# Optimization experiments

Hardware: AMD Instinct MI355X
Metric: run time of the kernel (lower is better)

The kernel has to match this reference:

```python
import jax, jax.numpy as jnp
import numpy as np

D_MODEL = 768
N_HEADS = 12
D_K = D_MODEL // N_HEADS


def setup_inputs() -> dict:
    key = jax.random.key(0)
    ks = jax.random.split(key, 11)
    B, T = 4, 2048
    s = 1.0 / np.sqrt(D_K)
    so = 1.0 / np.sqrt(D_MODEL)
    return {
        "q": jax.random.normal(ks[0], (B, T, D_MODEL), jnp.float32),
        "k": jax.random.normal(ks[1], (B, T, D_MODEL), jnp.float32),
        "v": jax.random.normal(ks[2], (B, T, D_MODEL), jnp.float32),
        "Wq": jax.random.normal(ks[3], (D_K, D_K), jnp.float32) * s,
        "bq": jax.random.normal(ks[4], (D_K,), jnp.float32) * s,
        "Wk": jax.random.normal(ks[5], (D_K, D_K), jnp.float32) * s,
        "bk": jax.random.normal(ks[6], (D_K,), jnp.float32) * s,
        "Wv": jax.random.normal(ks[7], (D_K, D_K), jnp.float32) * s,
        "bv": jax.random.normal(ks[8], (D_K,), jnp.float32) * s,
        "Wo": jax.random.normal(ks[9], (D_MODEL, D_MODEL), jnp.float32) * so,
        "bo": jax.random.normal(ks[10], (D_MODEL,), jnp.float32) * so,
    }


def reference(q, k, v, Wq, bq, Wk, bk, Wv, bv, Wo, bo):
    B, T, _ = q.shape
    # split into heads: [B, T, H, d_k]; per-head Linear shares weights across heads
    qh = q.reshape(B, T, N_HEADS, D_K)
    kh = k.reshape(B, T, N_HEADS, D_K)
    vh = v.reshape(B, T, N_HEADS, D_K)
    # torch Linear: x @ W^T + b, then transpose to [B, H, T, d_k]
    qh = jnp.einsum("bthd,ed->bhte", qh, Wq) + bq
    kh = jnp.einsum("bthd,ed->bhte", kh, Wk) + bk
    vh = jnp.einsum("bthd,ed->bhte", vh, Wv) + bv
    # scaled dot-product attention, full [B,H,T,T] scores (faithful to source)
    scores = jnp.einsum("bhqd,bhkd->bhqk", qh, kh) / jnp.sqrt(
        jnp.asarray(D_K, qh.dtype)
    )
    attn = jax.nn.softmax(scores, axis=-1)
    # einsum 'ijkl,ijlr->ikjr' -> output laid out [B, T, H, d_k]
    out_h = jnp.einsum("bhqk,bhkd->bqhd", attn, vh)
    concat = out_h.reshape(B, T, D_MODEL)
    return concat @ Wo.T + bo
```

## Files before the change

kernel.cpp:

```cpp
#include <hip/hip_runtime.h>
#include <hip/hip_bf16.h>


#define T_SEQ  2048
#define NH     12
#define DK     64
#define DMODEL 768
#define BATCH  4

typedef __attribute__((ext_vector_type(8))) short short8;
typedef __attribute__((ext_vector_type(4))) float f32x4;
typedef __attribute__((ext_vector_type(4))) unsigned short us4;
typedef __attribute__((ext_vector_type(2))) unsigned int u32x2;

__device__ __forceinline__ unsigned short f2bf(float f) {
  union { float f; unsigned int i; } x; x.f = f;
  unsigned int r = x.i + 0x7fffu + ((x.i >> 16) & 1u);
  return (unsigned short)(r >> 16);
}
__device__ __forceinline__ us4 f4_to_bf4(float4 v) {
  us4 r; r.x = f2bf(v.x); r.y = f2bf(v.y); r.z = f2bf(v.z); r.w = f2bf(v.w); return r;
}
__device__ __forceinline__ unsigned int pack_bf2(float a, float b) {
  union { __hip_bfloat162 h; unsigned int u; } x;
  x.h = __float22bfloat162_rn(float2{a, b});
  return x.u;
}


__global__ __launch_bounds__(256, 4)
void qkv_proj_kernel(const float* __restrict__ qin,
                     const float* __restrict__ kin,
                     const float* __restrict__ vin,
                     const float* __restrict__ Wq, const float* __restrict__ bq,
                     const float* __restrict__ Wk, const float* __restrict__ bk,
                     const float* __restrict__ Wv, const float* __restrict__ bv,
                     unsigned short* __restrict__ Qp,
                     unsigned short* __restrict__ Kp,
                     unsigned short* __restrict__ Vt)
{
  const int tt  = blockIdx.x;
  const int bh  = blockIdx.y;
  const int p   = blockIdx.z;
  const int b   = bh / NH, h = bh % NH;
  const int t0  = tt * 64;
  const int tid = threadIdx.x;
  const int wv  = tid >> 6;
  const int ln  = tid & 63;
  const int c   = ln & 15;
  const int qd  = ln >> 4;

  __shared__ __align__(16) unsigned short sX[64 * 72];
  __shared__ __align__(16) unsigned short sW[64 * 72];
  __shared__ __align__(16) unsigned short sVtr[64 * 68];

  const float* in = (p == 0) ? qin : (p == 1) ? kin : vin;
  const float* W  = (p == 0) ? Wq  : (p == 1) ? Wk  : Wv;
  const float* bs = (p == 0) ? bq  : (p == 1) ? bk  : bv;

  const int r0 = tid >> 4, g = tid & 15;
#pragma unroll
  for (int l = 0; l < 4; ++l) {
    int r = l * 16 + r0;
    float4 xv = *reinterpret_cast<const float4*>(in + ((size_t)(b * T_SEQ + t0 + r)) * DMODEL + h * DK + g * 4);
    *reinterpret_cast<us4*>(&sX[r * 72 + g * 4]) = f4_to_bf4(xv);
    float4 wvv = *reinterpret_cast<const float4*>(W + r * DK + g * 4);
    *reinterpret_cast<us4*>(&sW[r * 72 + g * 4]) = f4_to_bf4(wvv);
  }
  __syncthreads();

  short8 af[2];
#pragma unroll
  for (int kc = 0; kc < 2; ++kc)
    af[kc] = *reinterpret_cast<const short8*>(&sX[(wv * 16 + c) * 72 + kc * 32 + qd * 8]);

  f32x4 acc[4];
#pragma unroll
  for (int nb = 0; nb < 4; ++nb) {
    f32x4 a = {0.f, 0.f, 0.f, 0.f};
#pragma unroll
    for (int kc = 0; kc < 2; ++kc) {
      short8 bf = *reinterpret_cast<const short8*>(&sW[(nb * 16 + c) * 72 + kc * 32 + qd * 8]);
      a = __builtin_amdgcn_mfma_f32_16x16x32_bf16(af[kc], bf, a, 0, 0, 0);
    }
    acc[nb] = a;
  }

  const float cexp = 0.125f * 1.44269504088896340736f;
  if (p < 2) {
    unsigned short* outp = (p == 0) ? Qp : Kp;
    const float mul = (p == 0) ? cexp : 1.0f;
#pragma unroll
    for (int nb = 0; nb < 4; ++nb) {
      int n = nb * 16 + c;
      float bias = bs[n];
#pragma unroll
      for (int r = 0; r < 4; ++r) {
        int t = t0 + wv * 16 + qd * 4 + r;
        outp[((size_t)bh * T_SEQ + t) * DK + n] = f2bf((acc[nb][r] + bias) * mul);
      }
    }
  } else {
#pragma unroll
    for (int nb = 0; nb < 4; ++nb) {
      int n = nb * 16 + c;
      float bias = bs[n];
#pragma unroll
      for (int r = 0; r < 4; ++r) {
        int row = wv * 16 + qd * 4 + r;
        sVtr[n * 68 + row] = f2bf(acc[nb][r] + bias);
      }
    }
    __syncthreads();
#pragma unroll
    for (int l = 0; l < 4; ++l) {
      int d = l * 16 + r0;
      us4 val = *reinterpret_cast<const us4*>(&sVtr[d * 68 + g * 4]);
      *reinterpret_cast<us4*>(Vt + ((size_t)bh * DK + d) * T_SEQ + t0 + g * 4) = val;
    }
  }
}

__global__ __launch_bounds__(256, 4)
void flash_kernel(const unsigned short* __restrict__ Qp,
                  const unsigned short* __restrict__ Kp,
                  const unsigned short* __restrict__ Vt,
                  unsigned short* __restrict__ concat)
{
  const int qt  = blockIdx.x;
  const int bh  = blockIdx.y;
  const int b   = bh / NH, h = bh % NH;
  const int tid = threadIdx.x;
  const int wv  = tid >> 6;
  const int ln  = tid & 63;
  const int c   = ln & 15;
  const int qd  = ln >> 4;

  __shared__ __align__(16) unsigned short sK[64 * 72];
  __shared__ __align__(16) unsigned short sV[64 * 72];
  __shared__ __align__(16) unsigned short sP[4][2][16 * 72];

  const int row0 = qt * 128 + wv * 32;

  short8 qf[2][2];
#pragma unroll
  for (int f = 0; f < 2; ++f) {
    const unsigned short* qb = Qp + ((size_t)bh * T_SEQ + row0 + f * 16 + c) * DK + qd * 8;
    qf[f][0] = *reinterpret_cast<const short8*>(qb);
    qf[f][1] = *reinterpret_cast<const short8*>(qb + 32);
  }

  const int r0 = tid >> 4, g = tid & 15;
  us4 kreg[4], vreg[4];
#define LOAD_TILE(J)                                                                   \
  {                                                                                    \
    _Pragma("unroll")                                                                  \
    for (int l = 0; l < 4; ++l) {                                                      \
      int r = l * 16 + r0;                                                             \
      kreg[l] = *reinterpret_cast<const us4*>(Kp + ((size_t)bh * T_SEQ + (J) * 64 + r) * DK + g * 4); \
      vreg[l] = *reinterpret_cast<const us4*>(Vt + ((size_t)bh * DK + r) * T_SEQ + (J) * 64 + g * 4); \
    }                                                                                  \
  }

  LOAD_TILE(0);

  f32x4 o[2][4];
  float lsum[2] = {0.f, 0.f};
#pragma unroll
  for (int f = 0; f < 2; ++f)
#pragma unroll
    for (int nb = 0; nb < 4; ++nb) o[f][nb] = (f32x4){0.f, 0.f, 0.f, 0.f};

  for (int j = 0; j < T_SEQ / 64; ++j) {
    __syncthreads();
#pragma unroll
    for (int l = 0; l < 4; ++l) {
      int r = l * 16 + r0;
      *reinterpret_cast<us4*>(&sK[r * 72 + g * 4]) = kreg[l];
      *reinterpret_cast<us4*>(&sV[r * 72 + g * 4]) = vreg[l];
    }
    __syncthreads();

    int jn = (j + 1) & (T_SEQ / 64 - 1);
    LOAD_TILE(jn);

    short8 kf[4][2];
#pragma unroll
    for (int nb = 0; nb < 4; ++nb) {
      kf[nb][0] = *reinterpret_cast<const short8*>(&sK[(nb * 16 + c) * 72 + qd * 8]);
      kf[nb][1] = *reinterpret_cast<const short8*>(&sK[(nb * 16 + c) * 72 + 32 + qd * 8]);
    }

    f32x4 st[2][4];
#pragma unroll
    for (int f = 0; f < 2; ++f)
#pragma unroll
      for (int nb = 0; nb < 4; ++nb) {
        f32x4 a = {0.f, 0.f, 0.f, 0.f};
        a = __builtin_amdgcn_mfma_f32_16x16x32_bf16(kf[nb][0], qf[f][0], a, 0, 0, 0);
        a = __builtin_amdgcn_mfma_f32_16x16x32_bf16(kf[nb][1], qf[f][1], a, 0, 0, 0);
        st[f][nb] = a;
      }

#pragma unroll
    for (int f = 0; f < 2; ++f) {
#pragma unroll
      for (int nb = 0; nb < 4; ++nb) {
        float p0 = __builtin_amdgcn_exp2f(st[f][nb][0]);
        float p1 = __builtin_amdgcn_exp2f(st[f][nb][1]);
        float p2 = __builtin_amdgcn_exp2f(st[f][nb][2]);
        float p3 = __builtin_amdgcn_exp2f(st[f][nb][3]);
        lsum[f] += (p0 + p1) + (p2 + p3);
        u32x2 pku = {pack_bf2(p0, p1), pack_bf2(p2, p3)};
        *reinterpret_cast<us4*>(&sP[wv][f][c * 72 + nb * 16 + qd * 4]) =
            __builtin_bit_cast(us4, pku);
      }
    }

    short8 pf[2][2];
#pragma unroll
    for (int f = 0; f < 2; ++f) {
      pf[f][0] = *reinterpret_cast<const short8*>(&sP[wv][f][c * 72 + qd * 8]);
      pf[f][1] = *reinterpret_cast<const short8*>(&sP[wv][f][c * 72 + 32 + qd * 8]);
    }

    short8 vf[4][2];
#pragma unroll
    for (int nb = 0; nb < 4; ++nb) {
      vf[nb][0] = *reinterpret_cast<const short8*>(&sV[(nb * 16 + c) * 72 + qd * 8]);
      vf[nb][1] = *reinterpret_cast<const short8*>(&sV[(nb * 16 + c) * 72 + 32 + qd * 8]);
    }

#pragma unroll
    for (int f = 0; f < 2; ++f)
#pragma unroll
      for (int nb = 0; nb < 4; ++nb) {
        o[f][nb] = __builtin_amdgcn_mfma_f32_16x16x32_bf16(pf[f][0], vf[nb][0], o[f][nb], 0, 0, 0);
        o[f][nb] = __builtin_amdgcn_mfma_f32_16x16x32_bf16(pf[f][1], vf[nb][1], o[f][nb], 0, 0, 0);
      }
  }

  float linv[2];
#pragma unroll
  for (int f = 0; f < 2; ++f) {
    lsum[f] += __shfl_xor(lsum[f], 16, 64);
    lsum[f] += __shfl_xor(lsum[f], 32, 64);
    linv[f] = 1.0f / lsum[f];
  }

#pragma unroll
  for (int f = 0; f < 2; ++f) {
#pragma unroll
    for (int r = 0; r < 4; ++r) {
      float lr = __shfl(linv[f], qd * 4 + r, 16);
      int t = row0 + f * 16 + qd * 4 + r;
#pragma unroll
      for (int nb = 0; nb < 4; ++nb) {
        concat[((size_t)(b * T_SEQ + t)) * DMODEL + h * DK + nb * 16 + c] = f2bf(o[f][nb][r] * lr);
      }
    }
  }
#undef LOAD_TILE
}

__global__ __launch_bounds__(256, 3)
void oproj_kernel(const unsigned short* __restrict__ A,
                  const float* __restrict__ Wo,
                  const float* __restrict__ bo,
                  float* __restrict__ out)
{
  const int nt  = blockIdx.x;
  const int mt  = blockIdx.y;
  const int tid = threadIdx.x;
  const int wv  = tid >> 6;
  const int ln  = tid & 63;
  const int c   = ln & 15;
  const int qd  = ln >> 4;

  __shared__ __align__(16) unsigned short sA[128 * 136];
  __shared__ __align__(16) unsigned short sB[64 * 136];

  const int r16 = tid >> 4, g = tid & 15;
  short8 areg[8];
  float4 breg[4][2];
#define LOAD_K(KK)                                                                       \
  {                                                                                      \
    _Pragma("unroll")                                                                    \
    for (int l = 0; l < 8; ++l)                                                          \
      areg[l] = *reinterpret_cast<const short8*>(A + ((size_t)(mt * 128 + l * 16 + r16)) * DMODEL + (KK) * 128 + g * 8); \
    _Pragma("unroll")                                                                    \
    for (int l = 0; l < 4; ++l) {                                                        \
      const float* wp = Wo + ((size_t)(nt * 64 + l * 16 + r16)) * DMODEL + (KK) * 128 + g * 8; \
      breg[l][0] = *reinterpret_cast<const float4*>(wp);                                 \
      breg[l][1] = *reinterpret_cast<const float4*>(wp + 4);                             \
    }                                                                                    \
  }

  LOAD_K(0);

  f32x4 acc[2][4];
#pragma unroll
  for (int f = 0; f < 2; ++f)
#pragma unroll
    for (int nb = 0; nb < 4; ++nb) acc[f][nb] = (f32x4){0.f, 0.f, 0.f, 0.f};

  for (int kk = 0; kk < DMODEL / 128; ++kk) {
    __syncthreads();
#pragma unroll
    for (int l = 0; l < 8; ++l)
      *reinterpret_cast<short8*>(&sA[(l * 16 + r16) * 136 + g * 8]) = areg[l];
#pragma unroll
    for (int l = 0; l < 4; ++l) {
      *reinterpret_cast<us4*>(&sB[(l * 16 + r16) * 136 + g * 8]) = f4_to_bf4(breg[l][0]);
      *reinterpret_cast<us4*>(&sB[(l * 16 + r16) * 136 + g * 8 + 4]) = f4_to_bf4(breg[l][1]);
    }
    __syncthreads();

    int kn = kk + 1 < DMODEL / 128 ? kk + 1 : 0;
    LOAD_K(kn);

#pragma unroll
    for (int kc = 0; kc < 4; ++kc) {
      short8 af0 = *reinterpret_cast<const short8*>(&sA[(wv * 32 + c) * 136 + kc * 32 + qd * 8]);
      short8 af1 = *reinterpret_cast<const short8*>(&sA[(wv * 32 + 16 + c) * 136 + kc * 32 + qd * 8]);
#pragma unroll
      for (int nb = 0; nb < 4; ++nb) {
        short8 bfr = *reinterpret_cast<const short8*>(&sB[(nb * 16 + c) * 136 + kc * 32 + qd * 8]);
        acc[0][nb] = __builtin_amdgcn_mfma_f32_16x16x32_bf16(af0, bfr, acc[0][nb], 0, 0, 0);
        acc[1][nb] = __builtin_amdgcn_mfma_f32_16x16x32_bf16(af1, bfr, acc[1][nb], 0, 0, 0);
      }
    }
  }

#pragma unroll
  for (int f = 0; f < 2; ++f)
#pragma unroll
    for (int nb = 0; nb < 4; ++nb) {
      int n = nt * 64 + nb * 16 + c;
      float bias = bo[n];
#pragma unroll
      for (int r = 0; r < 4; ++r) {
        int m = mt * 128 + wv * 32 + f * 16 + qd * 4 + r;
        out[(size_t)m * DMODEL + n] = acc[f][nb][r] + bias;
      }
    }
#undef LOAD_K
}

extern "C" void kernel_launch(void* const* d_in, const int* in_sizes, int n_in,
                              void* d_out, int out_size, void* d_ws, size_t ws_size,
                              hipStream_t stream) {
  const float* q  = (const float*)d_in[0];
  const float* k  = (const float*)d_in[1];
  const float* v  = (const float*)d_in[2];
  const float* Wq = (const float*)d_in[3];
  const float* bq = (const float*)d_in[4];
  const float* Wk = (const float*)d_in[5];
  const float* bk = (const float*)d_in[6];
  const float* Wv = (const float*)d_in[7];
  const float* bv = (const float*)d_in[8];
  const float* Wo = (const float*)d_in[9];
  const float* bo = (const float*)d_in[10];

  const size_t NTOK = (size_t)BATCH * T_SEQ;
  const size_t PER  = NTOK * DK * NH;
  unsigned short* Qp     = (unsigned short*)d_ws;
  unsigned short* Kp     = Qp + PER;
  unsigned short* Vt     = Kp + PER;
  unsigned short* concat = Vt + PER;

  dim3 blk(256);
  qkv_proj_kernel<<<dim3(32, BATCH * NH, 3), blk, 0, stream>>>(q, k, v, Wq, bq, Wk, bk, Wv, bv, Qp, Kp, Vt);
  flash_kernel<<<dim3(16, BATCH * NH), blk, 0, stream>>>(Qp, Kp, Vt, concat);
  oproj_kernel<<<dim3(12, 64), blk, 0, stream>>>(concat, Wo, bo, (float*)d_out);
}
```

Measured before the change: 247.2 us.

## Loop QKV projection over four token tiles with register-prefetched inputs

Each QKV projection block now handles four 64-token tiles instead of one, loading and converting the weight matrix once and keeping its fragments in registers. The next tile's input is prefetched into registers while the current tile is computed. The float-to-bf16 conversion now uses the packed intrinsic, and launch bounds drop to 3 waves per SIMD for both the projection and flash kernels. The grid shrinks fourfold, which lowers parallelism, and the looser bounds may change flash-kernel register allocation and occupancy.

```diff
diff --git a/kernel.cpp b/kernel.cpp
--- a/kernel.cpp
+++ b/kernel.cpp
@@ -18,17 +18,18 @@
   unsigned int r = x.i + 0x7fffu + ((x.i >> 16) & 1u);
   return (unsigned short)(r >> 16);
 }
-__device__ __forceinline__ us4 f4_to_bf4(float4 v) {
-  us4 r; r.x = f2bf(v.x); r.y = f2bf(v.y); r.z = f2bf(v.z); r.w = f2bf(v.w); return r;
-}
 __device__ __forceinline__ unsigned int pack_bf2(float a, float b) {
   union { __hip_bfloat162 h; unsigned int u; } x;
   x.h = __float22bfloat162_rn(float2{a, b});
   return x.u;
 }
-
-
-__global__ __launch_bounds__(256, 4)
+__device__ __forceinline__ us4 f4_to_bf4(float4 v) {
+  u32x2 u = {pack_bf2(v.x, v.y), pack_bf2(v.z, v.w)};
+  return __builtin_bit_cast(us4, u);
+}
+
+
+__global__ __launch_bounds__(256, 3)
 void qkv_proj_kernel(const float* __restrict__ qin,
                      const float* __restrict__ kin,
                      const float* __restrict__ vin,
@@ -39,11 +40,10 @@
                      unsigned short* __restrict__ Kp,
                      unsigned short* __restrict__ Vt)
 {
-  const int tt  = blockIdx.x;
+  const int tg  = blockIdx.x;
   const int bh  = blockIdx.y;
   const int p   = blockIdx.z;
   const int b   = bh / NH, h = bh % NH;
-  const int t0  = tt * 64;
   const int tid = threadIdx.x;
   const int wv  = tid >> 6;
   const int ln  = tid & 63;
@@ -59,69 +59,91 @@
   const float* bs = (p == 0) ? bq  : (p == 1) ? bk  : bv;
 
   const int r0 = tid >> 4, g = tid & 15;
+
 #pragma unroll
   for (int l = 0; l < 4; ++l) {
     int r = l * 16 + r0;
-    float4 xv = *reinterpret_cast<const float4*>(in + ((size_t)(b * T_SEQ + t0 + r)) * DMODEL + h * DK + g * 4);
-    *reinterpret_cast<us4*>(&sX[r * 72 + g * 4]) = f4_to_bf4(xv);
     float4 wvv = *reinterpret_cast<const float4*>(W + r * DK + g * 4);
     *reinterpret_cast<us4*>(&sW[r * 72 + g * 4]) = f4_to_bf4(wvv);
   }
   __syncthreads();
-
-  short8 af[2];
-#pragma unroll
-  for (int kc = 0; kc < 2; ++kc)
-    af[kc] = *reinterpret_cast<const short8*>(&sX[(wv * 16 + c) * 72 + kc * 32 + qd * 8]);
-
-  f32x4 acc[4];
+  short8 wf[4][2];
 #pragma unroll
   for (int nb = 0; nb < 4; ++nb) {
-    f32x4 a = {0.f, 0.f, 0.f, 0.f};
-#pragma unroll
-    for (int kc = 0; kc < 2; ++kc) {
-      short8 bf = *reinterpret_cast<const short8*>(&sW[(nb * 16 + c) * 72 + kc * 32 + qd * 8]);
-      a = __builtin_amdgcn_mfma_f32_16x16x32_bf16(af[kc], bf, a, 0, 0, 0);
-    }
-    acc[nb] = a;
-  }
+    wf[nb][0] = *reinterpret_cast<const short8*>(&sW[(nb * 16 + c) * 72 + qd * 8]);
+    wf[nb][1] = *reinterpret_cast<const short8*>(&sW[(nb * 16 + c) * 72 + 32 + qd * 8]);
+  }
+
+  float4 xreg[4];
+#define LOAD_X(T0)                                                                     \
+  {                                                                                    \
+    _Pragma("unroll")                                                                  \
+    for (int l = 0; l < 4; ++l)                                                        \
+      xreg[l] = *reinterpret_cast<const float4*>(in + ((size_t)(b * T_SEQ + (T0) + l * 16 + r0)) * DMODEL + h * DK + g * 4); \
+  }
+
+  LOAD_X(tg * 256);
 
   const float cexp = 0.125f * 1.44269504088896340736f;
-  if (p < 2) {
-    unsigned short* outp = (p == 0) ? Qp : Kp;
-    const float mul = (p == 0) ? cexp : 1.0f;
+  const float mul  = (p == 0) ? cexp : 1.0f;
+
+  for (int it = 0; it < 4; ++it) {
+    const int t0 = tg * 256 + it * 64;
+    __syncthreads();
+#pragma unroll
+    for (int l = 0; l < 4; ++l)
+      *reinterpret_cast<us4*>(&sX[(l * 16 + r0) * 72 + g * 4]) = f4_to_bf4(xreg[l]);
+    __syncthreads();
+    if (it < 3) LOAD_X(t0 + 64);
+
+    short8 af0 = *reinterpret_cast<const short8*>(&sX[(wv * 16 + c) * 72 + qd * 8]);
+    short8 af1 = *reinterpret_cast<const short8*>(&sX[(wv * 16 + c) * 72 + 32 + qd * 8]);
+
+    f32x4 acc[4];
 #pragma unroll
     for (int nb = 0; nb < 4; ++nb) {
-      int n = nb * 16 + c;
-      float bias = bs[n];
-#pragma unroll
-      for (int r = 0; r < 4; ++r) {
-        int t = t0 + wv * 16 + qd * 4 + r;
-        outp[((size_t)bh * T_SEQ + t) * DK + n] = f2bf((acc[nb][r] + bias) * mul);
-      }
-    }
-  } else {
-#pragma unroll
-    for (int nb = 0; nb < 4; ++nb) {
-      int n = nb * 16 + c;
-      float bias = bs[n];
-#pragma unroll
-      for (int r = 0; r < 4; ++r) {
-        int row = wv * 16 + qd * 4 + r;
-        sVtr[n * 68 + row] = f2bf(acc[nb][r] + bias);
-      }
-    }
-    __syncthreads();
-#pragma unroll
-    for (int l = 0; l < 4; ++l) {
-      int d = l * 16 + r0;
-      us4 val = *reinterpret_cast<const us4*>(&sVtr[d * 68 + g * 4]);
-      *reinterpret_cast<us4*>(Vt + ((size_t)bh * DK + d) * T_SEQ + t0 + g * 4) = val;
-    }
-  }
-}
-
-__global__ __launch_bounds__(256, 4)
+      f32x4 a = {0.f, 0.f, 0.f, 0.f};
+      a = __builtin_amdgcn_mfma_f32_16x16x32_bf16(af0, wf[nb][0], a, 0, 0, 0);
+      a = __builtin_amdgcn_mfma_f32_16x16x32_bf16(af1, wf[nb][1], a, 0, 0, 0);
+      acc[nb] = a;
+    }
+
+    if (p < 2) {
+      unsigned short* outp = (p == 0) ? Qp : Kp;
+#pragma unroll
+      for (int nb = 0; nb < 4; ++nb) {
+        int n = nb * 16 + c;
+        float bias = bs[n];
+#pragma unroll
+        for (int r = 0; r < 4; ++r) {
+          int t = t0 + wv * 16 + qd * 4 + r;
+          outp[((size_t)bh * T_SEQ + t) * DK + n] = f2bf((acc[nb][r] + bias) * mul);
+        }
+      }
+    } else {
+#pragma unroll
+      for (int nb = 0; nb < 4; ++nb) {
+        int n = nb * 16 + c;
+        float bias = bs[n];
+#pragma unroll
+        for (int r = 0; r < 4; ++r) {
+          int row = wv * 16 + qd * 4 + r;
+          sVtr[n * 68 + row] = f2bf(acc[nb][r] + bias);
+        }
+      }
+      __syncthreads();
+#pragma unroll
+      for (int l = 0; l < 4; ++l) {
+        int d = l * 16 + r0;
+        us4 val = *reinterpret_cast<const us4*>(&sVtr[d * 68 + g * 4]);
+        *reinterpret_cast<us4*>(Vt + ((size_t)bh * DK + d) * T_SEQ + t0 + g * 4) = val;
+      }
+    }
+  }
+#undef LOAD_X
+}
+
+__global__ __launch_bounds__(256, 3)
 void flash_kernel(const unsigned short* __restrict__ Qp,
                   const unsigned short* __restrict__ Kp,
                   const unsigned short* __restrict__ Vt,
@@ -370,7 +392,7 @@
   unsigned short* concat = Vt + PER;
 
   dim3 blk(256);
-  qkv_proj_kernel<<<dim3(32, BATCH * NH, 3), blk, 0, stream>>>(q, k, v, Wq, bq, Wk, bk, Wv, bv, Qp, Kp, Vt);
+  qkv_proj_kernel<<<dim3(8, BATCH * NH, 3), blk, 0, stream>>>(q, k, v, Wq, bq, Wk, bk, Wv, bv, Qp, Kp, Vt);
   flash_kernel<<<dim3(16, BATCH * NH), blk, 0, stream>>>(Qp, Kp, Vt, concat);
   oproj_kernel<<<dim3(12, 64), blk, 0, stream>>>(concat, Wo, bo, (float*)d_out);
 }
```

Result: faster. 236.1 us (-4.5%).
